# Kernel tuning notes

Measured on AMD Instinct MI355X. Metric: run time of the kernel, lower is better.

## Reference

```python
import jax, jax.numpy as jnp
import numpy as np

N = 4_194_304          # number of samples
NUM_TIMES = 2048       # number of distinct (integer) event times


def setup_inputs() -> dict:
    key = jax.random.key(0)
    k1, k2, k3 = jax.random.split(key, 3)
    hazard_ratio = jax.random.normal(k1, (N, 1), dtype=jnp.float32)
    durations = jax.random.randint(k2, (N,), 0, NUM_TIMES, dtype=jnp.int32)
    events = jax.random.randint(k3, (N,), 0, 2, dtype=jnp.int32)
    return {"hazard_ratio": hazard_ratio, "durations": durations, "events": events}


def _cox_efron_loss(hazard_ratio, durations, events):
    """Vectorized Efron-tie Cox PH loss; same math as the nested-loop torch code.

    Original per unique event time t with n tied events:
        loss += sum_k hr_k  -  sum_{k=0}^{n-1} log( sum_{d_i>=t} e^{hr_i} - (k/n) * sum_{tied} e^{hr} )
    which we evaluate per-event-sample using its rank k among ties at its time.
    """
    hr = hazard_ratio.reshape(-1)                       # [N]  (squeeze(-1))
    e = events.astype(hr.dtype)                         # [N] 0/1 floats
    exp_hr = jnp.exp(hr)

    # Per-time aggregates (time ids are 0..NUM_TIMES-1)
    s = jax.ops.segment_sum(exp_hr, durations, num_segments=NUM_TIMES)        # sum e^hr at time d
    R = jnp.cumsum(s[::-1])[::-1]                                             # R[t] = sum_{d>=t} e^hr  (at-risk)
    T = jax.ops.segment_sum(exp_hr * e, durations, num_segments=NUM_TIMES)    # tied-event sum at time t
    n = jax.ops.segment_sum(e, durations, num_segments=NUM_TIMES)             # # tied events at time t

    # Rank of each event sample among the tied events at its time (0-indexed).
    order = jnp.argsort(durations)
    d_s = durations[order]
    e_s = e[order]
    cs = jnp.cumsum(e_s)                                # running event count
    is_start = jnp.concatenate([jnp.array([True]), d_s[1:] != d_s[:-1]])
    # cs - e_s at a segment start equals the event count before the segment;
    # carry it forward with a running max (offsets are nondecreasing, fillers are -1).
    start_val = jnp.where(is_start, cs - e_s, -1.0)
    offset = jax.lax.cummax(start_val)
    rank = cs - offset - 1.0                            # in {0..n-1} for event samples

    n_i = jnp.maximum(n[d_s], 1.0)                      # safe for non-event rows (masked below)
    corr = jnp.log(R[d_s] - (rank / n_i) * T[d_s])      # Efron correction term per event
    corr_sum = jnp.sum(jnp.where(e_s > 0, corr, 0.0))

    loss = jnp.sum(hr * e) - corr_sum
    return -loss / (jnp.sum(e) + 1e-7)


def reference(hazard_ratio, durations, events):
    return _cox_efron_loss(hazard_ratio, durations, events)
```

## Files before the change

kernel.cpp:

```cpp
#include <hip/hip_runtime.h>

#define NT 2048
#define HB 512
#define HT 1024
#define RB 128
#define RT 1024
#define EB 128
#define ET 1024

#define SC      4096.0f
#define INV_SC  (1.0 / 4096.0)
#define TM26    ((1u << 26) - 1)

typedef unsigned long long u64;
typedef unsigned u32;

__device__ __forceinline__ double wave_reduce(double v) {
#pragma unroll
    for (int o = 32; o > 0; o >>= 1) v += __shfl_down(v, o, 64);
    return v;
}

__global__ __launch_bounds__(HT) void k_hist(
    const float* __restrict__ hr, const int* __restrict__ dur,
    const int* __restrict__ ev, int n,
    u32* __restrict__ s0_part, u32* __restrict__ tn_part,
    double* __restrict__ hrE_part, double* __restrict__ eCnt_part,
    unsigned* __restrict__ counter)
{
    __shared__ u32    loc[2 * NT];
    __shared__ double redH[HT / 64], redC[HT / 64];

    const int tid = threadIdx.x, bid = blockIdx.x;
    if (bid == 0 && tid == 0) *counter = 0u;

    for (int i = tid; i < 2 * NT; i += HT) loc[i] = 0u;
    __syncthreads();

    float hrE = 0.f;
    int   ec  = 0;
    const int stride = HB * HT;
    const int nv = n >> 2;
    const float4* hr4 = (const float4*)hr;
    const int4*   d4p = (const int4*)dur;
    const int4*   e4p = (const int4*)ev;

    auto process = [&](const float4& h, const int4& d, const int4& e) {
        float hh[4] = { h.x, h.y, h.z, h.w };
        int   dd[4] = { d.x, d.y, d.z, d.w };
        int   ee[4] = { e.x, e.y, e.z, e.w };
#pragma unroll
        for (int u = 0; u < 4; ++u) {
            float eh = expf(hh[u]);
            u32 fx = (u32)(eh * SC + 0.5f);
            int idx = dd[u] + (ee[u] << 11);
            atomicAdd(&loc[idx], fx + ((u32)ee[u] << 26));
            hrE += hh[u] * (float)ee[u];
            ec  += ee[u];
        }
    };

    for (int i = bid * HT + tid; i < nv; i += 2 * stride) {
        const bool two = (i + stride) < nv;
        float4 h0 = hr4[i];
        int4   d0 = d4p[i];
        int4   e0 = e4p[i];
        float4 h1; int4 d1, e1;
        if (two) { h1 = hr4[i + stride]; d1 = d4p[i + stride]; e1 = e4p[i + stride]; }
        process(h0, d0, e0);
        if (two) process(h1, d1, e1);
    }
    for (int j = (nv << 2) + bid * HT + tid; j < n; j += stride) {
        float h = hr[j]; int d = dur[j]; int e = ev[j];
        float eh = expf(h);
        atomicAdd(&loc[d + (e << 11)], (u32)(eh * SC + 0.5f) + ((u32)e << 26));
        hrE += h * (float)e;
        ec  += e;
    }
    __syncthreads();

    const size_t base = (size_t)bid * NT;
    for (int k = tid; k < NT; k += HT) {
        s0_part[base + k] = loc[k];
        tn_part[base + k] = loc[NT + k];
    }

    double hrEd = wave_reduce((double)hrE);
    double ecd  = wave_reduce((double)ec);
    if ((tid & 63) == 0) { redH[tid >> 6] = hrEd; redC[tid >> 6] = ecd; }
    __syncthreads();
    if (tid == 0) {
        double hh = 0.0, cc = 0.0;
#pragma unroll
        for (int w = 0; w < HT / 64; ++w) { hh += redH[w]; cc += redC[w]; }
        hrE_part[bid]  = hh;
        eCnt_part[bid] = cc;
    }
}

__global__ __launch_bounds__(RT) void k_reduce(
    const u32* __restrict__ s0_part, const u32* __restrict__ tn_part,
    double* __restrict__ s_fin, double* __restrict__ T_fin,
    unsigned* __restrict__ n_fin)
{
    __shared__ u64      rs[64][16];
    __shared__ u64      rt[64][16];
    __shared__ unsigned rn[64][16];

    const int bi = threadIdx.x & 15;
    const int jg = threadIdx.x >> 4;
    const int t  = blockIdx.x * 16 + bi;

    u64 s = 0ull, T = 0ull;
    unsigned c = 0u;
#pragma unroll
    for (int m = 0; m < HB / 64; ++m) {
        int j = jg + (m << 6);
        size_t idx = (size_t)j * NT + t;
        s += s0_part[idx];
        u32 v = tn_part[idx];
        T += v & TM26;
        c += v >> 26;
    }
    rs[jg][bi] = s; rt[jg][bi] = T; rn[jg][bi] = c;
    __syncthreads();

    const int wv = threadIdx.x >> 6;
    const int l  = threadIdx.x & 63;
    u64 S  = rs[l][wv];
    u64 TT = rt[l][wv];
    u64 C  = rn[l][wv];
#pragma unroll
    for (int o = 32; o > 0; o >>= 1) {
        S  += __shfl_down(S,  o, 64);
        TT += __shfl_down(TT, o, 64);
        C  += __shfl_down(C,  o, 64);
    }
    if (l == 0) {
        int tt = blockIdx.x * 16 + wv;
        s_fin[tt] = (double)(S + TT) * INV_SC;
        T_fin[tt] = (double)TT * INV_SC;
        n_fin[tt] = (unsigned)C;
    }
}

__global__ __launch_bounds__(ET) void k_scan_efron_final(
    const double* __restrict__ s_fin, const double* __restrict__ T_fin,
    const unsigned* __restrict__ n_fin,
    double* __restrict__ corr_part, const double* __restrict__ hrE_part,
    const double* __restrict__ eCnt_part,
    unsigned* __restrict__ counter, float* __restrict__ out)
{
    __shared__ double sa[NT];
    __shared__ double sb[NT];
    __shared__ double red[16];
    __shared__ unsigned is_last;

    const int tid = threadIdx.x, bid = blockIdx.x;

    for (int i = tid; i < NT; i += ET) sa[i] = s_fin[i];
    __syncthreads();
    double* cur = sa;
    double* nxt = sb;
    for (int off = 1; off < NT; off <<= 1) {
        for (int i = tid; i < NT; i += ET) {
            double v = cur[i];
            if (i + off < NT) v += cur[i + off];
            nxt[i] = v;
        }
        __syncthreads();
        double* tmp = cur; cur = nxt; nxt = tmp;
    }

    const int wv = tid >> 6;
    const int l  = tid & 63;
    const int t  = bid * 16 + wv;
    unsigned nt = n_fin[t];
    double acc = 0.0;
    if (nt > 0) {
        double Rt = cur[t];
        double Tt = T_fin[t];
        double inv = 1.0 / (double)nt;
        for (unsigned k = l; k < nt; k += 64)
            acc += (double)logf((float)(Rt - (double)k * inv * Tt));
    }
    acc = wave_reduce(acc);
    if (l == 0) red[wv] = acc;
    __syncthreads();
    if (tid == 0) {
        double c = 0.0;
#pragma unroll
        for (int m = 0; m < 16; ++m) c += red[m];
        corr_part[bid] = c;
    }
    __syncthreads();

    if (tid == 0) {
        __threadfence();
        unsigned ticket = atomicAdd(counter, 1u);
        is_last = (ticket == EB - 1) ? 1u : 0u;
    }
    __syncthreads();
    if (is_last) {
        __threadfence();
        __shared__ double redA[16], redB[16], redC[16];
        double a = (tid < EB) ? corr_part[tid] : 0.0;
        double h = 0.0, c = 0.0;
        if (tid < HB) { h = hrE_part[tid]; c = eCnt_part[tid]; }
        a = wave_reduce(a); h = wave_reduce(h); c = wave_reduce(c);
        if ((tid & 63) == 0) { redA[tid >> 6] = a; redB[tid >> 6] = h; redC[tid >> 6] = c; }
        __syncthreads();
        if (tid == 0) {
            double A = 0.0, H = 0.0, C = 0.0;
#pragma unroll
            for (int w = 0; w < 16; ++w) { A += redA[w]; H += redB[w]; C += redC[w]; }
            out[0] = (float)(-(H - A) / (C + 1e-7));
        }
    }
}

extern "C" void kernel_launch(void* const* d_in, const int* in_sizes, int n_in,
                              void* d_out, int out_size, void* d_ws, size_t ws_size,
                              hipStream_t stream)
{
    const float* hr  = (const float*)d_in[0];
    const int*   dur = (const int*)d_in[1];
    const int*   ev  = (const int*)d_in[2];
    int n = in_sizes[1];

    char* ws = (char*)d_ws;
    u32*      s0_part   = (u32*)ws;
    u32*      tn_part   = (u32*)(ws + (size_t)4 * 1024 * 1024);
    char*     p         = ws + (size_t)8 * 1024 * 1024;
    double*   s_fin     = (double*)p;          p += NT * 8;
    double*   T_fin     = (double*)p;          p += NT * 8;
    unsigned* n_fin     = (unsigned*)p;        p += NT * 4;
    double*   corr_part = (double*)p;          p += EB * 8;
    double*   hrE_part  = (double*)p;          p += HB * 8;
    double*   eCnt_part = (double*)p;          p += HB * 8;
    unsigned* counter   = (unsigned*)p;

    hipLaunchKernelGGL(k_hist, dim3(HB), dim3(HT), 0, stream,
                       hr, dur, ev, n, s0_part, tn_part, hrE_part, eCnt_part, counter);
    hipLaunchKernelGGL(k_reduce, dim3(RB), dim3(RT), 0, stream,
                       s0_part, tn_part, s_fin, T_fin, n_fin);
    hipLaunchKernelGGL(k_scan_efron_final, dim3(EB), dim3(ET), 0, stream,
                       s_fin, T_fin, n_fin, corr_part, hrE_part, eCnt_part,
                       counter, (float*)d_out);
}
```

Baseline: 38.50 us.

## Halve histogram blocks, duplicate LDS histograms, prefetch loop, fast exp, retile reduce

Several changes at once. The histogram kernel uses half as many blocks, keeps two LDS histogram copies split by wave parity to cut atomic contention, replaces the two-way unrolled loop with a one-step register prefetch, and switches expf to __expf. The reduce kernel is retiled to 8 bins per block with a two-stage combine, matching the smaller partial buffer. Writing and reading fewer partials cuts global traffic, at the cost of a coarser grid, merge work for the duplicated histograms and slightly less accurate exp.

```diff
diff --git a/kernel.cpp b/kernel.cpp
--- a/kernel.cpp
+++ b/kernel.cpp
@@ -1,9 +1,9 @@
 #include <hip/hip_runtime.h>
 
 #define NT 2048
-#define HB 512
+#define HB 256
 #define HT 1024
-#define RB 128
+#define RB 256
 #define RT 1024
 #define EB 128
 #define ET 1024
@@ -28,14 +28,16 @@
     double* __restrict__ hrE_part, double* __restrict__ eCnt_part,
     unsigned* __restrict__ counter)
 {
-    __shared__ u32    loc[2 * NT];
+    __shared__ u32    loc[2][2 * NT];
     __shared__ double redH[HT / 64], redC[HT / 64];
 
     const int tid = threadIdx.x, bid = blockIdx.x;
     if (bid == 0 && tid == 0) *counter = 0u;
 
-    for (int i = tid; i < 2 * NT; i += HT) loc[i] = 0u;
-    __syncthreads();
+    for (int i = tid; i < 2 * NT; i += HT) { loc[0][i] = 0u; loc[1][i] = 0u; }
+    __syncthreads();
+
+    u32* img = loc[(tid >> 6) & 1];
 
     float hrE = 0.f;
     int   ec  = 0;
@@ -51,29 +53,34 @@
         int   ee[4] = { e.x, e.y, e.z, e.w };
 #pragma unroll
         for (int u = 0; u < 4; ++u) {
-            float eh = expf(hh[u]);
+            float eh = __expf(hh[u]);
             u32 fx = (u32)(eh * SC + 0.5f);
             int idx = dd[u] + (ee[u] << 11);
-            atomicAdd(&loc[idx], fx + ((u32)ee[u] << 26));
+            atomicAdd(&img[idx], fx + ((u32)ee[u] << 26));
             hrE += hh[u] * (float)ee[u];
             ec  += ee[u];
         }
     };
 
-    for (int i = bid * HT + tid; i < nv; i += 2 * stride) {
-        const bool two = (i + stride) < nv;
-        float4 h0 = hr4[i];
-        int4   d0 = d4p[i];
-        int4   e0 = e4p[i];
-        float4 h1; int4 d1, e1;
-        if (two) { h1 = hr4[i + stride]; d1 = d4p[i + stride]; e1 = e4p[i + stride]; }
-        process(h0, d0, e0);
-        if (two) process(h1, d1, e1);
+    int i = bid * HT + tid;
+    if (i < nv) {
+        float4 h_c = hr4[i];
+        int4   d_c = d4p[i];
+        int4   e_c = e4p[i];
+        for (i += stride; i < nv; i += stride) {
+            float4 h_n = hr4[i];
+            int4   d_n = d4p[i];
+            int4   e_n = e4p[i];
+            process(h_c, d_c, e_c);
+            h_c = h_n; d_c = d_n; e_c = e_n;
+        }
+        process(h_c, d_c, e_c);
     }
     for (int j = (nv << 2) + bid * HT + tid; j < n; j += stride) {
         float h = hr[j]; int d = dur[j]; int e = ev[j];
-        float eh = expf(h);
-        atomicAdd(&loc[d + (e << 11)], (u32)(eh * SC + 0.5f) + ((u32)e << 26));
+        float eh = __expf(h);
+        atomicAdd(&loc[(tid >> 6) & 1][d + (e << 11)],
+                  (u32)(eh * SC + 0.5f) + ((u32)e << 26));
         hrE += h * (float)e;
         ec  += e;
     }
@@ -81,8 +88,10 @@
 
     const size_t base = (size_t)bid * NT;
     for (int k = tid; k < NT; k += HT) {
-        s0_part[base + k] = loc[k];
-        tn_part[base + k] = loc[NT + k];
+        s0_part[base + k] = loc[0][k] + loc[1][k];
+        u32 a = loc[0][NT + k], b = loc[1][NT + k];
+        tn_part[base + k] = (((a >> 26) + (b >> 26)) << 26)
+                          + ((a & TM26) + (b & TM26));
     }
 
     double hrEd = wave_reduce((double)hrE);
@@ -103,19 +112,21 @@
     double* __restrict__ s_fin, double* __restrict__ T_fin,
     unsigned* __restrict__ n_fin)
 {
-    __shared__ u64      rs[64][16];
-    __shared__ u64      rt[64][16];
-    __shared__ unsigned rn[64][16];
-
-    const int bi = threadIdx.x & 15;
-    const int jg = threadIdx.x >> 4;
-    const int t  = blockIdx.x * 16 + bi;
+    __shared__ u64      rs[128][8];
+    __shared__ u64      rt[128][8];
+    __shared__ unsigned rn[128][8];
+    __shared__ u64      ps[8][2], pt[8][2];
+    __shared__ unsigned pn[8][2];
+
+    const int bi = threadIdx.x & 7;
+    const int jg = threadIdx.x >> 3;
+    const int t  = blockIdx.x * 8 + bi;
 
     u64 s = 0ull, T = 0ull;
     unsigned c = 0u;
 #pragma unroll
-    for (int m = 0; m < HB / 64; ++m) {
-        int j = jg + (m << 6);
+    for (int m = 0; m < HB / 128; ++m) {
+        int j = jg + (m << 7);
         size_t idx = (size_t)j * NT + t;
         s += s0_part[idx];
         u32 v = tn_part[idx];
@@ -125,22 +136,30 @@
     rs[jg][bi] = s; rt[jg][bi] = T; rn[jg][bi] = c;
     __syncthreads();
 
-    const int wv = threadIdx.x >> 6;
-    const int l  = threadIdx.x & 63;
-    u64 S  = rs[l][wv];
-    u64 TT = rt[l][wv];
-    u64 C  = rn[l][wv];
+    const int wv  = threadIdx.x >> 6;
+    const int l   = threadIdx.x & 63;
+    const int bin = wv >> 1;
+    const int hf  = wv & 1;
+    u64 S  = rs[hf * 64 + l][bin];
+    u64 TT = rt[hf * 64 + l][bin];
+    u64 C  = rn[hf * 64 + l][bin];
 #pragma unroll
     for (int o = 32; o > 0; o >>= 1) {
         S  += __shfl_down(S,  o, 64);
         TT += __shfl_down(TT, o, 64);
         C  += __shfl_down(C,  o, 64);
     }
-    if (l == 0) {
-        int tt = blockIdx.x * 16 + wv;
-        s_fin[tt] = (double)(S + TT) * INV_SC;
-        T_fin[tt] = (double)TT * INV_SC;
-        n_fin[tt] = (unsigned)C;
+    if (l == 0) { ps[bin][hf] = S; pt[bin][hf] = TT; pn[bin][hf] = (unsigned)C; }
+    __syncthreads();
+    if (threadIdx.x < 8) {
+        int b = threadIdx.x;
+        u64 S2  = ps[b][0] + ps[b][1];
+        u64 TT2 = pt[b][0] + pt[b][1];
+        unsigned C2 = pn[b][0] + pn[b][1];
+        int tt = blockIdx.x * 8 + b;
+        s_fin[tt] = (double)(S2 + TT2) * INV_SC;
+        T_fin[tt] = (double)TT2 * INV_SC;
+        n_fin[tt] = C2;
     }
 }
 
@@ -230,8 +249,8 @@
 
     char* ws = (char*)d_ws;
     u32*      s0_part   = (u32*)ws;
-    u32*      tn_part   = (u32*)(ws + (size_t)4 * 1024 * 1024);
-    char*     p         = ws + (size_t)8 * 1024 * 1024;
+    u32*      tn_part   = (u32*)(ws + (size_t)2 * 1024 * 1024);
+    char*     p         = ws + (size_t)4 * 1024 * 1024;
     double*   s_fin     = (double*)p;          p += NT * 8;
     double*   T_fin     = (double*)p;          p += NT * 8;
     unsigned* n_fin     = (unsigned*)p;        p += NT * 4;
```

New measurement: 35.86 us. 6.9% less time.
